# Kernel optimization log

Hardware: AMD Instinct MI355X
Metric: run time of the kernel (lower is better)

Reference implementation:

```python
import jax, jax.numpy as jnp
import numpy as np

EPS = 1e-8  # torch F.cosine_similarity norm clamp


def _l2norm(x):
    # normalize along last axis with torch-style eps clamp
    nrm = jnp.sqrt(jnp.sum(x * x, axis=-1))
    return x / jnp.maximum(nrm, EPS)[..., None]


def setup_inputs() -> dict:
    key = jax.random.key(0)
    k1, k2 = jax.random.split(key)
    n, c, h, w = 32, 64, 192, 192
    output = jax.random.normal(k1, (n, c, h, w), dtype=jnp.float32)
    target = jax.random.normal(k2, (n, c, h, w), dtype=jnp.float32)
    return {"output": output, "target": target}


def reference(output, target):
    n, c, h, w = output.shape
    # torch: output_h, _ = output.max(dim=-1)  -> values over width, shape (n,c,h)
    out_h = jnp.max(output, axis=-1)   # (n,c,h)
    out_w = jnp.max(output, axis=-2)   # (n,c,w)
    tgt_h = jnp.max(target, axis=-1)
    tgt_w = jnp.max(target, axis=-2)

    Po_h = jax.nn.softmax(out_h, axis=2)
    Pt_h = jax.nn.softmax(tgt_h, axis=2)
    Po_w = jax.nn.softmax(out_w, axis=2)
    Pt_w = jax.nn.softmax(tgt_w, axis=2)

    # normalize once; cosine sim = dot of unit vectors
    Ao_h, At_h = _l2norm(Po_h), _l2norm(Pt_h)
    Ao_w, At_w = _l2norm(Po_w), _l2norm(Pt_w)

    # positive (matched-channel) similarity, shape (n,c)
    h_sim_pos = jnp.sum(Ao_h * At_h, axis=2)
    w_sim_pos = jnp.sum(Ao_w * At_w, axis=2)
    sim_pos = 0.5 * (h_sim_pos + w_sim_pos)

    # full pairwise sum over all (i,j) channel pairs -> shape (n,)
    sim_h = jnp.einsum('nik,njk->n', Ao_h, At_h)
    sim_w = jnp.einsum('nik,njk->n', Ao_w, At_w)
    sim = 0.5 * (sim_h + sim_w)

    loss = -jnp.log(sim_pos / sim[:, None])  # (n,c)
    loss = loss / c / n
    return loss
```

## Files before the change

kernel.cpp:

```cpp
#include <hip/hip_runtime.h>
#include <math.h>

#define N_  32
#define C_  64
#define HW  192
#define NC  (N_ * C_)

__device__ __forceinline__ float wave_max(float v) {
#pragma unroll
    for (int off = 32; off; off >>= 1) v = fmaxf(v, __shfl_xor(v, off));
    return v;
}
__device__ __forceinline__ float wave_sum(float v) {
#pragma unroll
    for (int off = 32; off; off >>= 1) v += __shfl_xor(v, off);
    return v;
}

__device__ __forceinline__ float block_max(float v, float* red) {
    const int w = threadIdx.x >> 6, lane = threadIdx.x & 63;
    v = wave_max(v);
    if (lane == 0) red[w] = v;
    __syncthreads();
    float r = fmaxf(fmaxf(red[0], red[1]), fmaxf(red[2], red[3]));
    __syncthreads();
    return r;
}
__device__ __forceinline__ float block_sum(float v, float* red) {
    const int w = threadIdx.x >> 6, lane = threadIdx.x & 63;
    v = wave_sum(v);
    if (lane == 0) red[w] = v;
    __syncthreads();
    float r = (red[0] + red[1]) + (red[2] + red[3]);
    __syncthreads();
    return r;
}

#define FMAX4(a, v)                                                    \
    do {                                                               \
        (a).x = fmaxf((a).x, (v).x); (a).y = fmaxf((a).y, (v).y);      \
        (a).z = fmaxf((a).z, (v).z); (a).w = fmaxf((a).w, (v).w);      \
    } while (0)

__global__ __launch_bounds__(256) void k_stage1(const float* __restrict__ outp,
                                                const float* __restrict__ tgtp,
                                                float* __restrict__ simpos,
                                                float* __restrict__ Aout) {
    __shared__ float4 cpart[32][49];
    __shared__ float rowm[2][HW];
    __shared__ float colm[2][HW];
    __shared__ float A[4][HW];
    __shared__ float red[4];

    const int b   = blockIdx.x;
    const int tid = threadIdx.x;
    const int j   = tid & 7;
    const int r   = tid >> 3;
    const float NEG = -INFINITY;

    const float* X0 = outp + (size_t)b * (HW * HW);
    const float* X1 = tgtp + (size_t)b * (HW * HW);

    float4 cm0[6], cm1[6];
#pragma unroll
    for (int k = 0; k < 6; ++k) {
        cm0[k] = make_float4(NEG, NEG, NEG, NEG);
        cm1[k] = cm0[k];
    }

    for (int p = 0; p < 6; ++p) {
        const int row = p * 32 + r;
        const float4* r0 = (const float4*)(X0 + row * HW);
        const float4* r1 = (const float4*)(X1 + row * HW);
        float4 v0[6], v1[6];
#pragma unroll
        for (int k = 0; k < 6; ++k) v0[k] = r0[j + 8 * k];
#pragma unroll
        for (int k = 0; k < 6; ++k) v1[k] = r1[j + 8 * k];

        float rm0 = NEG, rm1 = NEG;
#pragma unroll
        for (int k = 0; k < 6; ++k) {
            FMAX4(cm0[k], v0[k]);
            FMAX4(cm1[k], v1[k]);
            rm0 = fmaxf(rm0, fmaxf(fmaxf(v0[k].x, v0[k].y), fmaxf(v0[k].z, v0[k].w)));
            rm1 = fmaxf(rm1, fmaxf(fmaxf(v1[k].x, v1[k].y), fmaxf(v1[k].z, v1[k].w)));
        }
#pragma unroll
        for (int off = 1; off < 8; off <<= 1) {
            rm0 = fmaxf(rm0, __shfl_xor(rm0, off));
            rm1 = fmaxf(rm1, __shfl_xor(rm1, off));
        }
        if (j == 0) { rowm[0][row] = rm0; rowm[1][row] = rm1; }
    }

    for (int t = 0; t < 2; ++t) {
        __syncthreads();
#pragma unroll
        for (int k = 0; k < 6; ++k) cpart[r][j + 8 * k] = t ? cm1[k] : cm0[k];
        __syncthreads();
        if (tid < HW) {
            const int c4 = tid >> 2, comp = tid & 3;
            float m = NEG;
#pragma unroll 4
            for (int rr = 0; rr < 32; ++rr) {
                m = fmaxf(m, ((const float*)&cpart[rr][c4])[comp]);
            }
            colm[t][tid] = m;
        }
    }
    __syncthreads();

    for (int v = 0; v < 4; ++v) {
        const float* src = (v == 0) ? rowm[0] : (v == 1) ? colm[0]
                         : (v == 2) ? rowm[1] : colm[1];
        float x = (tid < HW) ? src[tid] : NEG;
        float M = block_max(x, red);
        float e = (tid < HW) ? expf(x - M) : 0.0f;
        float ss = block_sum(e * e, red);
        if (tid < HW) A[v][tid] = e / sqrtf(ss);
    }
    __syncthreads();

    float pd = (tid < HW) ? (A[0][tid] * A[2][tid] + A[1][tid] * A[3][tid]) : 0.0f;
    float sp = block_sum(pd, red);
    if (tid == 0) simpos[b] = 0.5f * sp;

    float* dst = Aout + (size_t)b * 4 * HW;
    const float* Af = (const float*)A;
    for (int i = tid; i < 4 * HW; i += 256) dst[i] = Af[i];
}

__global__ __launch_bounds__(256) void k_stage2(const float* __restrict__ simpos,
                                                const float* __restrict__ Aout,
                                                float* __restrict__ loss) {
    __shared__ float S[4 * HW];
    __shared__ float red[4];
    const int n = blockIdx.x, tid = threadIdx.x;
    const float* base = Aout + (size_t)n * C_ * 4 * HW;

    float a0 = 0.0f, a1 = 0.0f, a2 = 0.0f;
    for (int c = 0; c < C_; ++c) {
        const float* a = base + c * 4 * HW;
        a0 += a[tid];
        a1 += a[tid + 256];
        a2 += a[tid + 512];
    }
    S[tid] = a0; S[tid + 256] = a1; S[tid + 512] = a2;
    __syncthreads();

    float p = 0.0f;
    if (tid < HW)
        p = S[0 * HW + tid] * S[2 * HW + tid] + S[1 * HW + tid] * S[3 * HW + tid];
    float sim = 0.5f * block_sum(p, red);

    if (tid < C_) {
        loss[n * C_ + tid] =
            -logf(simpos[n * C_ + tid] / sim) * (1.0f / (N_ * C_));
    }
}

extern "C" void kernel_launch(void* const* d_in, const int* in_sizes, int n_in,
                              void* d_out, int out_size, void* d_ws, size_t ws_size,
                              hipStream_t stream) {
    const float* outp = (const float*)d_in[0];
    const float* tgtp = (const float*)d_in[1];
    float* simpos = (float*)d_ws;
    float* Aout   = simpos + NC;
    float* lossp  = (float*)d_out;

    hipLaunchKernelGGL(k_stage1, dim3(NC), dim3(256), 0, stream,
                       outp, tgtp, simpos, Aout);
    hipLaunchKernelGGL(k_stage2, dim3(N_), dim3(256), 0, stream,
                       simpos, Aout, lossp);
}
```

Baseline: 576.4 us.

## Process tensors sequentially with register double-buffering and shuffle-based column max

Stage 1 now handles the output and target tiles one after the other instead of interleaved, which roughly halves live vector registers. Row loads are double-buffered in registers so the next row is prefetched while the current one is reduced. Column maxima are reduced across the wave with xor shuffles, leaving only a small 4-wave partial array in shared memory. This shrinks LDS use, and launch_bounds(256,4) requests higher occupancy, both aimed at better latency hiding on this memory-bound read. The cost is more shuffle instructions and less load parallelism across the two tensors within a thread.

```diff
diff --git a/kernel.cpp b/kernel.cpp
--- a/kernel.cpp
+++ b/kernel.cpp
@@ -42,70 +42,83 @@
         (a).z = fmaxf((a).z, (v).z); (a).w = fmaxf((a).w, (v).w);      \
     } while (0)
 
-__global__ __launch_bounds__(256) void k_stage1(const float* __restrict__ outp,
-                                                const float* __restrict__ tgtp,
-                                                float* __restrict__ simpos,
-                                                float* __restrict__ Aout) {
-    __shared__ float4 cpart[32][49];
+__global__ __launch_bounds__(256, 4) void k_stage1(const float* __restrict__ outp,
+                                                   const float* __restrict__ tgtp,
+                                                   float* __restrict__ simpos,
+                                                   float* __restrict__ Aout) {
+    __shared__ float4 cpart[4][8][6];
     __shared__ float rowm[2][HW];
     __shared__ float colm[2][HW];
     __shared__ float A[4][HW];
     __shared__ float red[4];
 
-    const int b   = blockIdx.x;
-    const int tid = threadIdx.x;
-    const int j   = tid & 7;
-    const int r   = tid >> 3;
+    const int b    = blockIdx.x;
+    const int tid  = threadIdx.x;
+    const int j    = tid & 7;
+    const int r8   = tid >> 3;
+    const int w    = tid >> 6;
     const float NEG = -INFINITY;
 
-    const float* X0 = outp + (size_t)b * (HW * HW);
-    const float* X1 = tgtp + (size_t)b * (HW * HW);
+    for (int t = 0; t < 2; ++t) {
+        const float* X = (t == 0 ? outp : tgtp) + (size_t)b * (HW * HW);
 
-    float4 cm0[6], cm1[6];
+        float4 cm[6];
 #pragma unroll
-    for (int k = 0; k < 6; ++k) {
-        cm0[k] = make_float4(NEG, NEG, NEG, NEG);
-        cm1[k] = cm0[k];
-    }
+        for (int k = 0; k < 6; ++k) cm[k] = make_float4(NEG, NEG, NEG, NEG);
 
-    for (int p = 0; p < 6; ++p) {
-        const int row = p * 32 + r;
-        const float4* r0 = (const float4*)(X0 + row * HW);
-        const float4* r1 = (const float4*)(X1 + row * HW);
-        float4 v0[6], v1[6];
+        float4 va[6];
 #pragma unroll
-        for (int k = 0; k < 6; ++k) v0[k] = r0[j + 8 * k];
+        for (int k = 0; k < 6; ++k)
+            va[k] = ((const float4*)(X + r8 * HW))[j + 8 * k];
+
 #pragma unroll
-        for (int k = 0; k < 6; ++k) v1[k] = r1[j + 8 * k];
+        for (int p = 0; p < 6; ++p) {
+            float4 vb[6];
+            if (p < 5) {
+                const float4* rp = (const float4*)(X + (p * 32 + 32 + r8) * HW);
+#pragma unroll
+                for (int k = 0; k < 6; ++k) vb[k] = rp[j + 8 * k];
+            }
+            float rm = NEG;
+#pragma unroll
+            for (int k = 0; k < 6; ++k) {
+                FMAX4(cm[k], va[k]);
+                rm = fmaxf(rm, fmaxf(fmaxf(va[k].x, va[k].y),
+                                     fmaxf(va[k].z, va[k].w)));
+            }
+#pragma unroll
+            for (int off = 1; off < 8; off <<= 1)
+                rm = fmaxf(rm, __shfl_xor(rm, off));
+            if (j == 0) rowm[t][p * 32 + r8] = rm;
+#pragma unroll
+            for (int k = 0; k < 6; ++k) va[k] = vb[k];
+        }
 
-        float rm0 = NEG, rm1 = NEG;
 #pragma unroll
-        for (int k = 0; k < 6; ++k) {
-            FMAX4(cm0[k], v0[k]);
-            FMAX4(cm1[k], v1[k]);
-            rm0 = fmaxf(rm0, fmaxf(fmaxf(v0[k].x, v0[k].y), fmaxf(v0[k].z, v0[k].w)));
-            rm1 = fmaxf(rm1, fmaxf(fmaxf(v1[k].x, v1[k].y), fmaxf(v1[k].z, v1[k].w)));
+        for (int off = 8; off < 64; off <<= 1) {
+#pragma unroll
+            for (int k = 0; k < 6; ++k) {
+                float4 o;
+                o.x = __shfl_xor(cm[k].x, off);
+                o.y = __shfl_xor(cm[k].y, off);
+                o.z = __shfl_xor(cm[k].z, off);
+                o.w = __shfl_xor(cm[k].w, off);
+                FMAX4(cm[k], o);
+            }
         }
+        __syncthreads();
+        if ((tid & 63) < 8) {
 #pragma unroll
-        for (int off = 1; off < 8; off <<= 1) {
-            rm0 = fmaxf(rm0, __shfl_xor(rm0, off));
-            rm1 = fmaxf(rm1, __shfl_xor(rm1, off));
+            for (int k = 0; k < 6; ++k) cpart[w][j][k] = cm[k];
         }
-        if (j == 0) { rowm[0][row] = rm0; rowm[1][row] = rm1; }
-    }
-
-    for (int t = 0; t < 2; ++t) {
-        __syncthreads();
-#pragma unroll
-        for (int k = 0; k < 6; ++k) cpart[r][j + 8 * k] = t ? cm1[k] : cm0[k];
         __syncthreads();
         if (tid < HW) {
-            const int c4 = tid >> 2, comp = tid & 3;
+            const int g = tid >> 2, comp = tid & 3;
+            const int jj = g & 7, kk = g >> 3;
             float m = NEG;
-#pragma unroll 4
-            for (int rr = 0; rr < 32; ++rr) {
-                m = fmaxf(m, ((const float*)&cpart[rr][c4])[comp]);
-            }
+#pragma unroll
+            for (int ww = 0; ww < 4; ++ww)
+                m = fmaxf(m, ((const float*)&cpart[ww][jj][kk])[comp]);
             colm[t][tid] = m;
         }
     }
```

Result: slower. 639.3 us (+10.9%).
